# Kernel optimization log

Hardware: AMD Instinct MI355X
Metric: run time of the kernel (lower is better)

## Reference

```python
import jax, jax.numpy as jnp
import numpy as np


def setup_inputs() -> dict:
    key = jax.random.key(0)
    ks = jax.random.split(key, 8)
    b, m, e, d = 8, 4096, 2048, 128
    features = jax.random.normal(ks[0], (b, m, d), dtype=jnp.float32)
    # sparse-ish binary incidence matrix (nodes x hyperedges)
    inc_mat = (jax.random.uniform(ks[1], (b, m, e)) < 0.02).astype(jnp.float32)
    s = 1.0 / np.sqrt(d)
    return {
        "features": features,
        "inc_mat": inc_mat,
        "vc_Wa": jax.random.uniform(ks[2], (d, d), minval=-s, maxval=s),
        "vc_Wp": jax.random.uniform(ks[3], (d, d), minval=-s, maxval=s),
        "vc_alpha": jnp.float32(0.5),
        "ec_Wa": jax.random.uniform(ks[4], (d, d), minval=-s, maxval=s),
        "ec_Wp": jax.random.uniform(ks[5], (d, d), minval=-s, maxval=s),
        "ec_alpha": jnp.float32(0.5),
        "n_layers": 3,
    }


def _vertex_conv(feat, inc, Wa, Wp, alpha, prev=None):
    # feat: [b,m,d], inc: [b,m,e]
    att = feat @ Wa.T                                   # [b,m,d]
    e_att = jnp.einsum('bme,bmd->bed', inc, att)        # inc^T @ att
    attw = jax.nn.softmax(e_att, axis=1)                # softmax over edges
    agg = jnp.einsum('bme,bmd->bed', inc, feat)         # collapsed bmed outer-product + contract
    ef = (agg * attw) @ Wp.T                            # [b,e,d]
    if prev is not None:
        ef = alpha * prev + (1.0 - alpha) * ef
    return ef


def _edge_conv(inc, edge_feats, Wa, Wp, alpha, prev=None):
    # NOTE: original EdgeConv computes softmax attention_weights but never uses them (dead code).
    w = jnp.einsum('bed,bme->bmd', edge_feats, inc)     # inc @ edge_feats
    nf = w @ Wp.T                                       # [b,m,d]
    if prev is not None:
        nf = alpha * prev + (1.0 - alpha) * nf
    return nf


def reference(features, inc_mat, vc_Wa, vc_Wp, vc_alpha, ec_Wa, ec_Wp, ec_alpha, n_layers):
    edge_feats = _vertex_conv(features, inc_mat, vc_Wa, vc_Wp, vc_alpha)
    node_feats = _edge_conv(inc_mat, edge_feats, ec_Wa, ec_Wp, ec_alpha)
    for _ in range(1, n_layers):
        edge_feats = _vertex_conv(features, inc_mat, vc_Wa, vc_Wp, vc_alpha, prev=edge_feats)
        node_feats = _edge_conv(inc_mat, edge_feats, ec_Wa, ec_Wp, ec_alpha, prev=node_feats)
    return node_feats, edge_feats
```

## Files before the change

### kernel.cpp

```cpp
#include <hip/hip_runtime.h>

#define BB 8
#define MM 4096
#define EE 2048
#define DD 128

typedef _Float16 f16x8 __attribute__((ext_vector_type(8)));
typedef float    f32x4 __attribute__((ext_vector_type(4)));

__global__ __launch_bounds__(256) void bitpack(const float* __restrict__ inc,
                                               unsigned long long* __restrict__ bits)
{
    const int wid  = (blockIdx.x * 256 + threadIdx.x) >> 6;
    const int lane = threadIdx.x & 63;
    const int nw   = (gridDim.x * 256) >> 6;
    const int total = BB * MM * (EE / 64);
    for (int w = wid; w < total; w += nw){
        float v = inc[(size_t)w * 64 + lane];
        unsigned long long m = __ballot(v != 0.0f);
        if (lane == 0) bits[w] = m;
    }
}

__global__ __launch_bounds__(256) void bit_transpose(const unsigned long long* __restrict__ bits,
                                                     unsigned long long* __restrict__ bitsT)
{
    const int b = blockIdx.z;
    const int w = threadIdx.x >> 6;
    const int lane = threadIdx.x & 63;
    const int m0 = (blockIdx.y * 4 + w) * 64;
    const int e0 = blockIdx.x * 64;
    unsigned long long v = bits[((size_t)b * MM + m0 + lane) * (EE / 64) + (e0 >> 6)];
    unsigned long long mine = 0;
    #pragma unroll
    for (int e = 0; e < 64; e++){
        unsigned long long bal = __ballot((v >> e) & 1ull);
        if (lane == e) mine = bal;
    }
    bitsT[((size_t)b * EE + e0 + lane) * (MM / 64) + (m0 >> 6)] = mine;
}

__global__ __launch_bounds__(256) void transpose_to16(const float* __restrict__ src,
                                                      _Float16* __restrict__ dst,
                                                      int R, int C)
{
    __shared__ alignas(16) float tile[64 * 67];
    const int tilesC = C >> 6;
    const int r0 = (blockIdx.x / tilesC) << 6;
    const int c0 = (blockIdx.x % tilesC) << 6;
    const float* s = src + (size_t)blockIdx.y * R * C;
    _Float16*   d = dst + (size_t)blockIdx.y * R * C;
    const int t = threadIdx.x;
    #pragma unroll
    for (int i = 0; i < 4; i++){
        int idx = t + 256 * i;
        int r = idx >> 4, c4 = idx & 15;
        float4 v = *(const float4*)(s + (size_t)(r0 + r) * C + c0 + c4 * 4);
        tile[(c4 * 4 + 0) * 67 + r] = v.x;
        tile[(c4 * 4 + 1) * 67 + r] = v.y;
        tile[(c4 * 4 + 2) * 67 + r] = v.z;
        tile[(c4 * 4 + 3) * 67 + r] = v.w;
    }
    __syncthreads();
    #pragma unroll
    for (int i = 0; i < 2; i++){
        int idx = t + 256 * i;
        int row = idx >> 3, rb = idx & 7;
        f16x8 h;
        #pragma unroll
        for (int j = 0; j < 8; j++) h[j] = (_Float16)tile[row * 67 + rb * 8 + j];
        *(f16x8*)(d + (size_t)(c0 + row) * R + r0 + rb * 8) = h;
    }
}

__global__ __launch_bounds__(256) void bitgemm(const uint4* __restrict__ bitsrc,
                                               const _Float16* __restrict__ dense,
                                               float* __restrict__ out,
                                               int R, int Ktot, int Kslice,
                                               unsigned sliceStride)
{
    __shared__ alignas(16) char smem[69632];
    _Float16* lD0 = (_Float16*)smem;
    _Float16* lD1 = (_Float16*)(smem + 32768);
    uint4* lB0 = (uint4*)(smem + 65536);
    uint4* lB1 = (uint4*)(smem + 65536 + 2048);

    const int b = blockIdx.y;
    const int row0 = blockIdx.x * 128;
    const int PB = Ktot >> 7;
    const uint4* bp = bitsrc + (size_t)b * R * PB + (size_t)row0 * PB;
    const _Float16* dp = dense + (size_t)b * 128 * Ktot;
    float* op = out + (size_t)blockIdx.z * sliceStride
                    + (size_t)b * R * 128 + (size_t)row0 * 128;

    const int kbase = blockIdx.z * Kslice;
    const int nchunk = Kslice >> 7;

    const int t = threadIdx.x;
    const int lane = t & 63;
    const int w = t >> 6;
    const int fr = lane & 15, q = lane >> 4;
    const int q8 = q * 8;

    f32x4 acc[2][8] = {};
    uint4 rd[8];
    uint4 rb;

    auto loadg = [&](int kg){
        #pragma unroll
        for (int i = 0; i < 8; i++){
            int idx = t + 256 * i;
            int dd = idx >> 4, kb = idx & 15;
            rd[i] = *(const uint4*)(dp + (size_t)dd * Ktot + kg + kb * 8);
        }
        if (t < 128) rb = bp[(size_t)t * PB + (kg >> 7)];
    };
    auto stage = [&](int buf){
        _Float16* lD = buf ? lD1 : lD0;
        uint4* lB = buf ? lB1 : lB0;
        #pragma unroll
        for (int i = 0; i < 8; i++){
            int idx = t + 256 * i;
            int dd = idx >> 4, kb = idx & 15;
            *(uint4*)&lD[dd * 128 + ((kb ^ (dd & 7)) * 8)] = rd[i];
        }
        if (t < 128) lB[t] = rb;
    };
    auto compute = [&](int buf){
        const _Float16* lD = buf ? lD1 : lD0;
        const uint4* lB = buf ? lB1 : lB0;
        uint4 bw[2];
        #pragma unroll
        for (int r = 0; r < 2; r++)
            bw[r] = lB[w * 32 + r * 16 + fr];
        #pragma unroll
        for (int h = 0; h < 4; h++){
            f16x8 af[2];
            #pragma unroll
            for (int r = 0; r < 2; r++){
                unsigned word = ((const unsigned*)&bw[r])[h];
                unsigned byte = (word >> q8) & 0xFFu;
                #pragma unroll
                for (int j = 0; j < 8; j++)
                    af[r][j] = (_Float16)(float)((byte >> j) & 1u);
            }
            #pragma unroll
            for (int c = 0; c < 8; c++){
                int row = c * 16 + fr;
                f16x8 bf = *(const f16x8*)&lD[row * 128 + (((h * 4 + q) ^ (row & 7)) * 8)];
                #pragma unroll
                for (int r = 0; r < 2; r++)
                    acc[r][c] = __builtin_amdgcn_mfma_f32_16x16x32_f16(af[r], bf, acc[r][c], 0, 0, 0);
            }
        }
    };

    loadg(kbase);
    stage(0);
    __syncthreads();
    for (int c = 0; c < nchunk; c++){
        if (c + 1 < nchunk) loadg(kbase + (c + 1) * 128);
        compute(c & 1);
        if (c + 1 < nchunk) stage((c + 1) & 1);
        __syncthreads();
    }
    float* sT = (float*)smem;
    #pragma unroll
    for (int r = 0; r < 2; r++)
        #pragma unroll
        for (int c = 0; c < 8; c++)
            #pragma unroll
            for (int reg = 0; reg < 4; reg++)
                sT[(w * 32 + r * 16 + q * 4 + reg) * 132 + c * 16 + fr] = acc[r][c][reg];
    __syncthreads();
    #pragma unroll
    for (int i = 0; i < 16; i++){
        int idx = t + 256 * i;
        int row = idx >> 5, c4 = idx & 31;
        float4 v = *(const float4*)&sT[row * 132 + c4 * 4];
        *(float4*)(op + (size_t)row * 128 + c4 * 4) = v;
    }
}

__global__ __launch_bounds__(256) void addred(const float4* __restrict__ a,
                                              const float4* __restrict__ bsrc,
                                              float4* __restrict__ o, int n4)
{
    int i = blockIdx.x * 256 + threadIdx.x;
    int st = gridDim.x * 256;
    for (; i < n4; i += st){
        float4 x = a[i], y = bsrc[i];
        o[i] = make_float4(x.x + y.x, x.y + y.y, x.z + y.z, x.w + y.w);
    }
}

__global__ __launch_bounds__(256) void wc_mm(const float* __restrict__ eWp,
                                             const float* __restrict__ vWp,
                                             float* __restrict__ Wc)
{
    int i = blockIdx.x * 2 + (threadIdx.x >> 7);
    int j = threadIdx.x & 127;
    float acc = 0.f;
    for (int k = 0; k < 128; k++)
        acc += eWp[i * 128 + k] * vWp[k * 128 + j];
    Wc[i * 128 + j] = acc;
}

__global__ __launch_bounds__(256) void rowmm(const float* A,
                                             const float* __restrict__ W,
                                             float* C)
{
    __shared__ alignas(16) float lA[32][132];
    __shared__ alignas(16) float lW[64][140];
    const int t = threadIdx.x;
    const int row0 = blockIdx.x * 32;
    const float4* A4 = (const float4*)A;
    const float4* W4 = (const float4*)W;

    #pragma unroll
    for (int i = 0; i < 4; i++){
        int idx = t + 256 * i;
        int r = idx >> 5, k4 = idx & 31;
        *(float4*)&lA[r][k4 * 4] = A4[(size_t)(row0 + r) * 32 + k4];
    }
    const int qq = t >> 5;
    const int cc = t & 31;

    #pragma unroll
    for (int ph = 0; ph < 2; ph++){
        __syncthreads();
        #pragma unroll
        for (int i = 0; i < 8; i++){
            int idx = t + 256 * i;
            int c = idx >> 5, k4 = idx & 31;
            *(float4*)&lW[c][k4 * 4] = W4[(size_t)(ph * 64 + c) * 32 + k4];
        }
        __syncthreads();
        float s[4][2] = {};
        for (int k4 = 0; k4 < 32; k4++){
            float4 w0 = *(const float4*)&lW[cc][k4 * 4];
            float4 w1 = *(const float4*)&lW[cc + 32][k4 * 4];
            #pragma unroll
            for (int j = 0; j < 4; j++){
                float4 a = *(const float4*)&lA[qq + 8 * j][k4 * 4];
                s[j][0] += a.x * w0.x + a.y * w0.y + a.z * w0.z + a.w * w0.w;
                s[j][1] += a.x * w1.x + a.y * w1.y + a.z * w1.z + a.w * w1.w;
            }
        }
        #pragma unroll
        for (int j = 0; j < 4; j++){
            size_t ro = (size_t)(row0 + qq + 8 * j) * DD + ph * 64;
            C[ro + cc]      = s[j][0];
            C[ro + cc + 32] = s[j][1];
        }
    }
}

__global__ __launch_bounds__(256) void sm_part(const float* __restrict__ eatt,
                                               float* __restrict__ part)
{
    const int b = blockIdx.x, slab = blockIdx.y;
    const int t = threadIdx.x;
    const int dl = t & 127, eh = t >> 7;
    const size_t base = (size_t)b * EE * DD + dl;
    const int e0 = slab * 256;
    float m = -1e30f;
    for (int s = 0; s < 128; s++)
        m = fmaxf(m, eatt[base + (size_t)(e0 + eh + 2 * s) * DD]);
    float l = 0.f;
    for (int s = 0; s < 128; s++)
        l += __expf(eatt[base + (size_t)(e0 + eh + 2 * s) * DD] - m);
    __shared__ float red[2][128][2];
    red[eh][dl][0] = m; red[eh][dl][1] = l;
    __syncthreads();
    if (t < 128){
        float m0 = red[0][t][0], l0 = red[0][t][1];
        float m1 = red[1][t][0], l1 = red[1][t][1];
        float M = fmaxf(m0, m1);
        float L = l0 * __expf(m0 - M) + l1 * __expf(m1 - M);
        float* p = part + ((size_t)(b * 8 + slab) * DD + t) * 2;
        p[0] = M; p[1] = L;
    }
}

__global__ __launch_bounds__(256) void sm_apply(float* __restrict__ eatt,
                                                const float* __restrict__ agg,
                                                const float* __restrict__ part)
{
    const int b = blockIdx.x, sl = blockIdx.y;
    const int t = threadIdx.x;
    __shared__ float mv[128], iv[128];
    if (t < 128){
        float mbuf[8], lbuf[8];
        float M = -1e30f;
        #pragma unroll
        for (int s = 0; s < 8; s++){
            const float* p = part + ((size_t)(b * 8 + s) * DD + t) * 2;
            mbuf[s] = p[0]; lbuf[s] = p[1];
            M = fmaxf(M, mbuf[s]);
        }
        float L = 0.f;
        #pragma unroll
        for (int s = 0; s < 8; s++) L += lbuf[s] * __expf(mbuf[s] - M);
        mv[t] = M; iv[t] = 1.f / L;
    }
    __syncthreads();
    const int dl = t & 127, eh = t >> 7;
    const size_t base = (size_t)b * EE * DD + dl;
    const int e0 = sl * 128;
    for (int s = 0; s < 64; s++){
        size_t ix = base + (size_t)(e0 + eh + 2 * s) * DD;
        eatt[ix] = agg[ix] * __expf(eatt[ix] - mv[dl]) * iv[dl];
    }
}

extern "C" void kernel_launch(void* const* d_in, const int* in_sizes, int n_in,
                              void* d_out, int out_size, void* d_ws, size_t ws_size,
                              hipStream_t stream)
{
    const float* feat = (const float*)d_in[0];
    const float* inc  = (const float*)d_in[1];
    const float* vWa  = (const float*)d_in[2];
    const float* vWp  = (const float*)d_in[3];
    const float* eWp  = (const float*)d_in[6];

    float* node_out = (float*)d_out;
    float* edge_out = node_out + (size_t)BB * MM * DD;

    float* p0    = node_out + 2097152;
    _Float16* featT = (_Float16*)node_out;
    float* agg   = node_out;
    float* eattP = node_out + 2097152;
    float* part  = edge_out;

    char* w = (char*)d_ws;
    unsigned long long* bits  = (unsigned long long*)w;
    unsigned long long* bitsT = (unsigned long long*)(w + ((size_t)8 << 20));
    _Float16* PT = (_Float16*)(w + ((size_t)8 << 20));
    float* Wc = (float*)(w + ((size_t)12 << 20));

    dim3 blk(256);

    bitpack<<<dim3(2048), blk, 0, stream>>>(inc, bits);
    bit_transpose<<<dim3(EE / 64, MM / 256, BB), blk, 0, stream>>>(bits, bitsT);
    transpose_to16<<<dim3((MM / 64) * (DD / 64), BB), blk, 0, stream>>>(feat, featT, MM, DD);
    bitgemm<<<dim3(EE / 128, BB, 2), blk, 0, stream>>>(
        (const uint4*)bitsT, featT, p0, EE, MM, 2048, 2097152u);
    addred<<<dim3(1024), blk, 0, stream>>>(
        (const float4*)p0, (const float4*)(p0 + 2097152), (float4*)agg, 524288);
    rowmm<<<dim3(BB * EE / 32), blk, 0, stream>>>(agg, vWa, eattP);
    sm_part <<<dim3(BB, 8),  blk, 0, stream>>>(eattP, part);
    sm_apply<<<dim3(BB, 16), blk, 0, stream>>>(eattP, agg, part);
    rowmm<<<dim3(BB * EE / 32), blk, 0, stream>>>(eattP, vWp, edge_out);
    transpose_to16<<<dim3((EE / 64) * (DD / 64), BB), blk, 0, stream>>>(eattP, PT, EE, DD);
    wc_mm<<<dim3(64), blk, 0, stream>>>(eWp, vWp, Wc);
    bitgemm<<<dim3(MM / 128, BB, 1), blk, 0, stream>>>(
        (const uint4*)bits, PT, node_out, MM, EE, 2048, 0u);
    rowmm<<<dim3(BB * MM / 32), blk, 0, stream>>>(node_out, Wc, node_out);
}
```

Baseline: 634.8 us.

## Retile bitgemm to 64-wide K chunks, 4-way split-K, fuse partial-sum reduction into rowmm

```diff
diff --git a/kernel.cpp b/kernel.cpp
--- a/kernel.cpp
+++ b/kernel.cpp
@@ -9,16 +9,23 @@
 typedef float    f32x4 __attribute__((ext_vector_type(4)));
 
 __global__ __launch_bounds__(256) void bitpack(const float* __restrict__ inc,
-                                               unsigned long long* __restrict__ bits)
-{
-    const int wid  = (blockIdx.x * 256 + threadIdx.x) >> 6;
-    const int lane = threadIdx.x & 63;
-    const int nw   = (gridDim.x * 256) >> 6;
-    const int total = BB * MM * (EE / 64);
-    for (int w = wid; w < total; w += nw){
-        float v = inc[(size_t)w * 64 + lane];
-        unsigned long long m = __ballot(v != 0.0f);
-        if (lane == 0) bits[w] = m;
+                                               unsigned* __restrict__ bits32)
+{
+    const size_t total32 = (size_t)BB * MM * EE / 32;
+    size_t i  = (size_t)blockIdx.x * 256 + threadIdx.x;
+    size_t st = (size_t)gridDim.x * 256;
+    for (; i < total32; i += st){
+        const float4* p = (const float4*)(inc + i * 32);
+        unsigned u = 0;
+        #pragma unroll
+        for (int j = 0; j < 8; j++){
+            float4 v = p[j];
+            u |= (v.x != 0.f) ? (1u << (j * 4 + 0)) : 0u;
+            u |= (v.y != 0.f) ? (1u << (j * 4 + 1)) : 0u;
+            u |= (v.z != 0.f) ? (1u << (j * 4 + 2)) : 0u;
+            u |= (v.w != 0.f) ? (1u << (j * 4 + 3)) : 0u;
+        }
+        bits32[i] = u;
     }
 }
 
@@ -73,72 +80,66 @@
     }
 }
 
-__global__ __launch_bounds__(256) void bitgemm(const uint4* __restrict__ bitsrc,
+template<int RF>
+__global__ __launch_bounds__(256) void bitgemm(const uint2* __restrict__ bitrows,
                                                const _Float16* __restrict__ dense,
                                                float* __restrict__ out,
                                                int R, int Ktot, int Kslice,
                                                unsigned sliceStride)
 {
-    __shared__ alignas(16) char smem[69632];
-    _Float16* lD0 = (_Float16*)smem;
-    _Float16* lD1 = (_Float16*)(smem + 32768);
-    uint4* lB0 = (uint4*)(smem + 65536);
-    uint4* lB1 = (uint4*)(smem + 65536 + 2048);
+    constexpr int TR = RF * 64;
+    constexpr int SM = (32768 + 2 * TR * 8) > 33792 ? (32768 + 2 * TR * 8) : 33792;
+    __shared__ alignas(16) char smem[SM];
 
     const int b = blockIdx.y;
-    const int row0 = blockIdx.x * 128;
-    const int PB = Ktot >> 7;
-    const uint4* bp = bitsrc + (size_t)b * R * PB + (size_t)row0 * PB;
+    const int row0 = blockIdx.x * TR;
+    const int WB = Ktot >> 6;
+    const uint2* bp = bitrows + ((size_t)b * R + row0) * WB;
     const _Float16* dp = dense + (size_t)b * 128 * Ktot;
-    float* op = out + (size_t)blockIdx.z * sliceStride
-                    + (size_t)b * R * 128 + (size_t)row0 * 128;
-
+    float* op = out + (size_t)blockIdx.z * sliceStride + ((size_t)b * R + row0) * 128;
     const int kbase = blockIdx.z * Kslice;
-    const int nchunk = Kslice >> 7;
-
-    const int t = threadIdx.x;
-    const int lane = t & 63;
-    const int w = t >> 6;
-    const int fr = lane & 15, q = lane >> 4;
-    const int q8 = q * 8;
-
-    f32x4 acc[2][8] = {};
-    uint4 rd[8];
-    uint4 rb;
+    const int nchunk = Kslice >> 6;
+
+    const int t = threadIdx.x, lane = t & 63, w = t >> 6;
+    const int fr = lane & 15, q = lane >> 4, q8 = q * 8;
+
+    f32x4 acc[RF][8] = {};
+    uint4 rd[4];
+    uint2 rb;
 
     auto loadg = [&](int kg){
         #pragma unroll
-        for (int i = 0; i < 8; i++){
+        for (int i = 0; i < 4; i++){
             int idx = t + 256 * i;
-            int dd = idx >> 4, kb = idx & 15;
+            int dd = idx >> 3, kb = idx & 7;
             rd[i] = *(const uint4*)(dp + (size_t)dd * Ktot + kg + kb * 8);
         }
-        if (t < 128) rb = bp[(size_t)t * PB + (kg >> 7)];
+        if (t < TR) rb = bp[(size_t)t * WB + (kg >> 6)];
     };
     auto stage = [&](int buf){
-        _Float16* lD = buf ? lD1 : lD0;
-        uint4* lB = buf ? lB1 : lB0;
-        #pragma unroll
-        for (int i = 0; i < 8; i++){
+        _Float16* lD = (_Float16*)(smem + buf * 16384);
+        uint2* lB = (uint2*)(smem + 32768 + buf * TR * 8);
+        #pragma unroll
+        for (int i = 0; i < 4; i++){
             int idx = t + 256 * i;
-            int dd = idx >> 4, kb = idx & 15;
-            *(uint4*)&lD[dd * 128 + ((kb ^ (dd & 7)) * 8)] = rd[i];
-        }
-        if (t < 128) lB[t] = rb;
+            int dd = idx >> 3, kb = idx & 7;
+            *(uint4*)&lD[dd * 64 + ((kb ^ (dd & 7)) * 8)] = rd[i];
+        }
+        if (t < TR) lB[t] = rb;
     };
     auto compute = [&](int buf){
-        const _Float16* lD = buf ? lD1 : lD0;
-        const uint4* lB = buf ? lB1 : lB0;
-        uint4 bw[2];
-        #pragma unroll
-        for (int r = 0; r < 2; r++)
-            bw[r] = lB[w * 32 + r * 16 + fr];
-        #pragma unroll
-        for (int h = 0; h < 4; h++){
-            f16x8 af[2];
+        const _Float16* lD = (const _Float16*)(smem + buf * 16384);
+        const uint2* lB = (const uint2*)(smem + 32768 + buf * TR * 8);
+        uint2 bw[RF];
+        #pragma unroll
+        for (int r = 0; r < RF; r++)
+            bw[r] = lB[w * (RF * 16) + r * 16 + fr];
+        #pragma unroll
+        for (int h = 0; h < 2; h++){
+            f16x8 af[RF];
             #pragma unroll
-            for (int r = 0; r < 2; r++){
-                unsigned word = ((const unsigned*)&bw[r])[h];
+            for (int r = 0; r < RF; r++){
+                unsigned word = h ? bw[r].y : bw[r].x;
                 unsigned byte = (word >> q8) & 0xFFu;
                 #pragma unroll
                 for (int j = 0; j < 8; j++)
@@ -146,10 +147,10 @@
             }
             #pragma unroll
             for (int c = 0; c < 8; c++){
-                int row = c * 16 + fr;
-                f16x8 bf = *(const f16x8*)&lD[row * 128 + (((h * 4 + q) ^ (row & 7)) * 8)];
+                int drow = c * 16 + fr;
+                f16x8 bf = *(const f16x8*)&lD[drow * 64 + (((h * 4 + q) ^ (drow & 7)) * 8)];
                 #pragma unroll
-                for (int r = 0; r < 2; r++)
+                for (int r = 0; r < RF; r++)
                     acc[r][c] = __builtin_amdgcn_mfma_f32_16x16x32_f16(af[r], bf, acc[r][c], 0, 0, 0);
             }
         }
@@ -159,69 +160,62 @@
     stage(0);
     __syncthreads();
     for (int c = 0; c < nchunk; c++){
-        if (c + 1 < nchunk) loadg(kbase + (c + 1) * 128);
+        if (c + 1 < nchunk) loadg(kbase + (c + 1) * 64);
         compute(c & 1);
         if (c + 1 < nchunk) stage((c + 1) & 1);
         __syncthreads();
     }
+
     float* sT = (float*)smem;
     #pragma unroll
-    for (int r = 0; r < 2; r++)
-        #pragma unroll
-        for (int c = 0; c < 8; c++)
-            #pragma unroll
-            for (int reg = 0; reg < 4; reg++)
-                sT[(w * 32 + r * 16 + q * 4 + reg) * 132 + c * 16 + fr] = acc[r][c][reg];
-    __syncthreads();
-    #pragma unroll
-    for (int i = 0; i < 16; i++){
-        int idx = t + 256 * i;
-        int row = idx >> 5, c4 = idx & 31;
-        float4 v = *(const float4*)&sT[row * 132 + c4 * 4];
-        *(float4*)(op + (size_t)row * 128 + c4 * 4) = v;
-    }
-}
-
-__global__ __launch_bounds__(256) void addred(const float4* __restrict__ a,
-                                              const float4* __restrict__ bsrc,
-                                              float4* __restrict__ o, int n4)
-{
-    int i = blockIdx.x * 256 + threadIdx.x;
-    int st = gridDim.x * 256;
-    for (; i < n4; i += st){
-        float4 x = a[i], y = bsrc[i];
-        o[i] = make_float4(x.x + y.x, x.y + y.y, x.z + y.z, x.w + y.w);
-    }
-}
-
-__global__ __launch_bounds__(256) void wc_mm(const float* __restrict__ eWp,
-                                             const float* __restrict__ vWp,
-                                             float* __restrict__ Wc)
-{
-    int i = blockIdx.x * 2 + (threadIdx.x >> 7);
-    int j = threadIdx.x & 127;
-    float acc = 0.f;
-    for (int k = 0; k < 128; k++)
-        acc += eWp[i * 128 + k] * vWp[k * 128 + j];
-    Wc[i * 128 + j] = acc;
-}
-
-__global__ __launch_bounds__(256) void rowmm(const float* A,
-                                             const float* __restrict__ W,
-                                             float* C)
+    for (int hh = 0; hh < RF; hh++){
+        __syncthreads();
+        #pragma unroll
+        for (int r = 0; r < RF; r++){
+            int rowbase = w * (RF * 16) + r * 16;
+            if (rowbase >= hh * 64 && rowbase < hh * 64 + 64){
+                #pragma unroll
+                for (int c = 0; c < 8; c++)
+                    #pragma unroll
+                    for (int reg = 0; reg < 4; reg++)
+                        sT[(rowbase - hh * 64 + q * 4 + reg) * 132 + c * 16 + fr] = acc[r][c][reg];
+            }
+        }
+        __syncthreads();
+        #pragma unroll
+        for (int i = 0; i < 8; i++){
+            int idx = t + 256 * i;
+            int lrow = idx >> 5, c4 = idx & 31;
+            float4 v = *(const float4*)&sT[lrow * 132 + c4 * 4];
+            *(float4*)(op + (size_t)(hh * 64 + lrow) * 128 + c4 * 4) = v;
+        }
+    }
+}
+
+__global__ __launch_bounds__(256) void rowmm_sum4(const float* __restrict__ p,
+                                                  const float* __restrict__ W,
+                                                  float* aggOut,
+                                                  float* __restrict__ C)
 {
     __shared__ alignas(16) float lA[32][132];
     __shared__ alignas(16) float lW[64][140];
     const int t = threadIdx.x;
     const int row0 = blockIdx.x * 32;
-    const float4* A4 = (const float4*)A;
+    const float4* P4 = (const float4*)p;
     const float4* W4 = (const float4*)W;
+    float4* A4 = (float4*)aggOut;
+    const size_t SS = 2097152 / 4;
 
     #pragma unroll
     for (int i = 0; i < 4; i++){
         int idx = t + 256 * i;
         int r = idx >> 5, k4 = idx & 31;
-        *(float4*)&lA[r][k4 * 4] = A4[(size_t)(row0 + r) * 32 + k4];
+        size_t gi = (size_t)(row0 + r) * 32 + k4;
+        float4 a = P4[gi], b = P4[gi + SS], c = P4[gi + 2 * SS], d = P4[gi + 3 * SS];
+        float4 s = make_float4(a.x + b.x + c.x + d.x, a.y + b.y + c.y + d.y,
+                               a.z + b.z + c.z + d.z, a.w + b.w + c.w + d.w);
+        *(float4*)&lA[r][k4 * 4] = s;
+        A4[gi] = s;
     }
     const int qq = t >> 5;
     const int cc = t & 31;
@@ -254,6 +248,68 @@
             C[ro + cc + 32] = s[j][1];
         }
     }
+}
+
+__global__ __launch_bounds__(256) void rowmm(const float* A,
+                                             const float* __restrict__ W,
+                                             float* C)
+{
+    __shared__ alignas(16) float lA[32][132];
+    __shared__ alignas(16) float lW[64][140];
+    const int t = threadIdx.x;
+    const int row0 = blockIdx.x * 32;
+    const float4* A4 = (const float4*)A;
+    const float4* W4 = (const float4*)W;
+
+    #pragma unroll
+    for (int i = 0; i < 4; i++){
+        int idx = t + 256 * i;
+        int r = idx >> 5, k4 = idx & 31;
+        *(float4*)&lA[r][k4 * 4] = A4[(size_t)(row0 + r) * 32 + k4];
+    }
+    const int qq = t >> 5;
+    const int cc = t & 31;
+
+    #pragma unroll
+    for (int ph = 0; ph < 2; ph++){
+        __syncthreads();
+        #pragma unroll
+        for (int i = 0; i < 8; i++){
+            int idx = t + 256 * i;
+            int c = idx >> 5, k4 = idx & 31;
+            *(float4*)&lW[c][k4 * 4] = W4[(size_t)(ph * 64 + c) * 32 + k4];
+        }
+        __syncthreads();
+        float s[4][2] = {};
+        for (int k4 = 0; k4 < 32; k4++){
+            float4 w0 = *(const float4*)&lW[cc][k4 * 4];
+            float4 w1 = *(const float4*)&lW[cc + 32][k4 * 4];
+            #pragma unroll
+            for (int j = 0; j < 4; j++){
+                float4 a = *(const float4*)&lA[qq + 8 * j][k4 * 4];
+                s[j][0] += a.x * w0.x + a.y * w0.y + a.z * w0.z + a.w * w0.w;
+                s[j][1] += a.x * w1.x + a.y * w1.y + a.z * w1.z + a.w * w1.w;
+            }
+        }
+        #pragma unroll
+        for (int j = 0; j < 4; j++){
+            size_t ro = (size_t)(row0 + qq + 8 * j) * DD + ph * 64;
+            C[ro + cc]      = s[j][0];
+            C[ro + cc + 32] = s[j][1];
+        }
+    }
+}
+
+__global__ __launch_bounds__(256) void wc_mm(const float* __restrict__ eWp,
+                                             const float* __restrict__ vWp,
+                                             float* __restrict__ Wc)
+{
+    int i = blockIdx.x * 2 + (threadIdx.x >> 7);
+    int j = threadIdx.x & 127;
+    float acc = 0.f;
+    for (int k = 0; k < 128; k++)
+        acc += eWp[i * 128 + k] * vWp[k * 128 + j];
+    Wc[i * 128 + j] = acc;
 }
 
 __global__ __launch_bounds__(256) void sm_part(const float* __restrict__ eatt,
@@ -278,8 +334,8 @@
         float m1 = red[1][t][0], l1 = red[1][t][1];
         float M = fmaxf(m0, m1);
         float L = l0 * __expf(m0 - M) + l1 * __expf(m1 - M);
-        float* p = part + ((size_t)(b * 8 + slab) * DD + t) * 2;
-        p[0] = M; p[1] = L;
+        float* pp = part + ((size_t)(b * 8 + slab) * DD + t) * 2;
+        pp[0] = M; pp[1] = L;
     }
 }
 
@@ -295,8 +351,8 @@
         float M = -1e30f;
         #pragma unroll
         for (int s = 0; s < 8; s++){
-            const float* p = part + ((size_t)(b * 8 + s) * DD + t) * 2;
-            mbuf[s] = p[0]; lbuf[s] = p[1];
+            const float* pp = part + ((size_t)(b * 8 + s) * DD + t) * 2;
+            mbuf[s] = pp[0]; lbuf[s] = pp[1];
             M = fmaxf(M, mbuf[s]);
         }
         float L = 0.f;
@@ -327,34 +383,33 @@
     float* node_out = (float*)d_out;
     float* edge_out = node_out + (size_t)BB * MM * DD;
 
-    float* p0    = node_out + 2097152;
+    char* w = (char*)d_ws;
+    unsigned* bits32 = (unsigned*)w;
+    unsigned long long* bits = (unsigned long long*)w;
+    unsigned long long* bitsT = (unsigned long long*)(w + ((size_t)8 << 20));
+    _Float16* PT = (_Float16*)(w + ((size_t)8 << 20));
+    float* pk = (float*)(w + ((size_t)16 << 20));
+    float* agg = pk;
+    float* Wc = (float*)(w + ((size_t)48 << 20));
+
     _Float16* featT = (_Float16*)node_out;
-    float* agg   = node_out;
     float* eattP = node_out + 2097152;
     float* part  = edge_out;
 
-    char* w = (char*)d_ws;
-    unsigned long long* bits  = (unsigned long long*)w;
-    unsigned long long* bitsT = (unsigned long long*)(w + ((size_t)8 << 20));
-    _Float16* PT = (_Float16*)(w + ((size_t)8 << 20));
-    float* Wc = (float*)(w + ((size_t)12 << 20));
-
     dim3 blk(256);
 
-    bitpack<<<dim3(2048), blk, 0, stream>>>(inc, bits);
+    bitpack<<<dim3(4096), blk, 0, stream>>>(inc, bits32);
     bit_transpose<<<dim3(EE / 64, MM / 256, BB), blk, 0, stream>>>(bits, bitsT);
     transpose_to16<<<dim3((MM / 64) * (DD / 64), BB), blk, 0, stream>>>(feat, featT, MM, DD);
-    bitgemm<<<dim3(EE / 128, BB, 2), blk, 0, stream>>>(
-        (const uint4*)bitsT, featT, p0, EE, MM, 2048, 2097152u);
-    addred<<<dim3(1024), blk, 0, stream>>>(
-        (const float4*)p0, (const float4*)(p0 + 2097152), (float4*)agg, 524288);
-    rowmm<<<dim3(BB * EE / 32), blk, 0, stream>>>(agg, vWa, eattP);
+    bitgemm<2><<<dim3(EE / 128, BB, 4), blk, 0, stream>>>(
+        (const uint2*)bitsT, featT, pk, EE, MM, 1024, 2097152u);
+    rowmm_sum4<<<dim3(BB * EE / 32), blk, 0, stream>>>(pk, vWa, agg, eattP);
     sm_part <<<dim3(BB, 8),  blk, 0, stream>>>(eattP, part);
     sm_apply<<<dim3(BB, 16), blk, 0, stream>>>(eattP, agg, part);
     rowmm<<<dim3(BB * EE / 32), blk, 0, stream>>>(eattP, vWp, edge_out);
     transpose_to16<<<dim3((EE / 64) * (DD / 64), BB), blk, 0, stream>>>(eattP, PT, EE, DD);
     wc_mm<<<dim3(64), blk, 0, stream>>>(eWp, vWp, Wc);
-    bitgemm<<<dim3(MM / 128, BB, 1), blk, 0, stream>>>(
-        (const uint4*)bits, PT, node_out, MM, EE, 2048, 0u);
+    bitgemm<1><<<dim3(MM / 64, BB, 1), blk, 0, stream>>>(
+        (const uint2*)bits, PT, node_out, MM, EE, 2048, 0u);
     rowmm<<<dim3(BB * MM / 32), blk, 0, stream>>>(node_out, Wc, node_out);
 }
```

Result: slower. 660.9 us (+4.1%).
